# Performance work log

Measured on AMD Instinct MI355X. Metric: run time of the kernel, lower is better.

## Reference

```python
import jax, jax.numpy as jnp
import numpy as np
import math

N = 100000      # nodes
E = 1600000     # edges
F_IN = 256      # num_features
H = 64          # num_hidden
C = 64          # num_classes
L = 8           # num_layers
ALPHA = 0.5
THETA = 1.0


def setup_inputs() -> dict:
    key = jax.random.key(0)
    ks = jax.random.split(key, 7)
    x = jax.random.normal(ks[0], (N, F_IN), dtype=jnp.float32)
    edge_index = jax.random.randint(ks[1], (2, E), 0, N, dtype=jnp.int64)
    w_in = jax.random.normal(ks[2], (F_IN, H), dtype=jnp.float32) / np.float32(math.sqrt(F_IN))
    b_in = jnp.zeros((H,), dtype=jnp.float32)
    w_layers = jax.random.normal(ks[3], (L, H, H), dtype=jnp.float32) / np.float32(math.sqrt(H))
    w_out = jax.random.normal(ks[4], (H, C), dtype=jnp.float32) / np.float32(math.sqrt(H))
    b_out = jnp.zeros((C,), dtype=jnp.float32)
    return {"x": x, "edge_index": edge_index, "w_in": w_in, "b_in": b_in,
            "w_layers": w_layers, "w_out": w_out, "b_out": b_out}


def reference(x, edge_index, w_in, b_in, w_layers, w_out, b_out):
    # --- gcn_norm: add self loops, symmetric D^-1/2 (A+I) D^-1/2 ---
    loop = jnp.arange(N, dtype=edge_index.dtype)
    src = jnp.concatenate([edge_index[0], loop])   # [E+N]
    dst = jnp.concatenate([edge_index[1], loop])   # [E+N]
    deg = jax.ops.segment_sum(jnp.ones_like(src, dtype=x.dtype), dst, num_segments=N)
    dinv = jnp.where(deg > 0, jax.lax.rsqrt(jnp.maximum(deg, 1e-12)), 0.0)
    norm = dinv[src] * dinv[dst]                   # [E+N]

    # initial linear + ELU (dropout is identity in eval mode)
    h = jax.nn.elu(x @ w_in + b_in)                # [N, H]
    x0 = h

    for l in range(L):
        beta = math.log(THETA / (l + 1) + 1.0)     # GCN2Conv beta, layer index 1-based
        # sparse neighbor aggregation: P_hat @ h
        agg = jax.ops.segment_sum(norm[:, None] * h[src], dst, num_segments=N)  # [N, H]
        s = (1.0 - ALPHA) * agg + ALPHA * x0       # initial residual
        out = (1.0 - beta) * s + beta * (s @ w_layers[l])  # identity mapping (shared weights)
        h = jax.nn.elu(out) + out                  # elu + residual (dropout off)

    return h @ w_out + b_out                       # [N, C]
```

## Files before the change

kernel.cpp:

```cpp
#include <hip/hip_runtime.h>
#include <hip/hip_fp16.h>
#include <math.h>

#define NN 100000
#define EE 1600000
#define HH 64
#define LL 8
#define NBLK ((NN + 1023) / 1024)
#define AGG3_BLOCKS ((NN + 31) / 32)

#define NPB 512
#define BSH 9
#define NBUCK ((NN + NPB - 1) / NPB)
#define BIN_CHUNK 4096

typedef _Float16 f16x8 __attribute__((ext_vector_type(8)));
typedef float f32x4 __attribute__((ext_vector_type(4)));

__device__ __forceinline__ float eluf(float x) { return x > 0.0f ? x : expm1f(x); }


__global__ void count_edges_v2(const int* __restrict__ dst, int* __restrict__ counts) {
    int i = blockIdx.x * blockDim.x + threadIdx.x;
    if (i < EE) atomicAdd(&counts[dst[i]], 1);
}

__global__ void scan_block_v2(const int* __restrict__ counts, int* __restrict__ rp,
                              int* __restrict__ partial, float* __restrict__ dinv) {
    __shared__ int sm[256];
    const int t = threadIdx.x;
    const int base = blockIdx.x * 1024 + t * 4;
    int v0 = 0, v1 = 0, v2 = 0, v3 = 0;
    if (base + 0 < NN) v0 = counts[base + 0];
    if (base + 1 < NN) v1 = counts[base + 1];
    if (base + 2 < NN) v2 = counts[base + 2];
    if (base + 3 < NN) v3 = counts[base + 3];
    if (base + 0 < NN) dinv[base + 0] = rsqrtf((float)(v0 + 1));
    if (base + 1 < NN) dinv[base + 1] = rsqrtf((float)(v1 + 1));
    if (base + 2 < NN) dinv[base + 2] = rsqrtf((float)(v2 + 1));
    if (base + 3 < NN) dinv[base + 3] = rsqrtf((float)(v3 + 1));
    const int s = v0 + v1 + v2 + v3;
    sm[t] = s;
    __syncthreads();
    for (int off = 1; off < 256; off <<= 1) {
        int x = 0;
        if (t >= off) x = sm[t - off];
        __syncthreads();
        if (t >= off) sm[t] += x;
        __syncthreads();
    }
    int excl = sm[t] - s;
    if (t == 255) partial[blockIdx.x] = sm[255];
    if (base + 0 < NN) rp[base + 0] = excl;
    excl += v0;
    if (base + 1 < NN) rp[base + 1] = excl;
    excl += v1;
    if (base + 2 < NN) rp[base + 2] = excl;
    excl += v2;
    if (base + 3 < NN) rp[base + 3] = excl;
}

__global__ void scan_top_v2(int* partial) {
    __shared__ int sm[128];
    const int t = threadIdx.x;
    const int v = (t < NBLK) ? partial[t] : 0;
    sm[t] = v;
    __syncthreads();
    for (int off = 1; off < 128; off <<= 1) {
        int x = 0;
        if (t >= off) x = sm[t - off];
        __syncthreads();
        if (t >= off) sm[t] += x;
        __syncthreads();
    }
    if (t < NBLK) partial[t] = sm[t] - v;
}

__global__ void scan_add_v2(int* rp, const int* __restrict__ partial) {
    const int i = blockIdx.x * blockDim.x + threadIdx.x;
    if (i < NN) rp[i] += partial[i >> 10];
    else if (i == NN) rp[NN] = EE;
}


__global__ __launch_bounds__(256) void bin_edges_v1(const int* __restrict__ src,
                                                    const int* __restrict__ dst,
                                                    const int* __restrict__ rp,
                                                    int* __restrict__ bfill,
                                                    unsigned* __restrict__ tmp) {
    __shared__ int hist[NBUCK];
    __shared__ int basei[NBUCK];
    __shared__ int rpb[NBUCK];
    __shared__ int cur[NBUCK];
    const int t = threadIdx.x;
    const int e0 = blockIdx.x * BIN_CHUNK;
    for (int b = t; b < NBUCK; b += 256) {
        hist[b] = 0;
        cur[b] = 0;
    }
    __syncthreads();
    int myd[16];
#pragma unroll
    for (int i = 0; i < 16; ++i) {
        const int e = e0 + i * 256 + t;
        int d = -1;
        if (e < EE) {
            d = dst[e];
            atomicAdd(&hist[d >> BSH], 1);
        }
        myd[i] = d;
    }
    __syncthreads();
    for (int b = t; b < NBUCK; b += 256) {
        const int h = hist[b];
        basei[b] = h ? atomicAdd(&bfill[b], h) : 0;
        rpb[b] = rp[b << BSH];
    }
    __syncthreads();
#pragma unroll
    for (int i = 0; i < 16; ++i) {
        const int e = e0 + i * 256 + t;
        if (e < EE) {
            const int d = myd[i];
            const int b = d >> BSH;
            const int slot = atomicAdd(&cur[b], 1);
            tmp[rpb[b] + basei[b] + slot] =
                ((unsigned)(d & (NPB - 1)) << 17) | (unsigned)src[e];
        }
    }
}

__global__ __launch_bounds__(512) void unbin_v1(const unsigned* __restrict__ tmp,
                                                const int* __restrict__ rp,
                                                int* __restrict__ col) {
    __shared__ int lrp[NPB];
    __shared__ int lfill[NPB];
    const int t = threadIdx.x;
    const int node0 = blockIdx.x << BSH;
    const int nodes = (NN - node0 < NPB) ? (NN - node0) : NPB;
    for (int i = t; i < nodes; i += 512) {
        lrp[i] = rp[node0 + i];
        lfill[i] = 0;
    }
    __syncthreads();
    const int lo = rp[node0];
    const int hi = rp[node0 + nodes];
    for (int e = lo + t; e < hi; e += 512) {
        const unsigned v = tmp[e];
        const int s = (int)(v & 0x1FFFFu);
        const int doff = (int)(v >> 17);
        const int pos = lrp[doff] + atomicAdd(&lfill[doff], 1);
        col[pos] = s;
    }
}

__global__ void init_sent_v2(__half* a, __half* b) {
    const int t = threadIdx.x;
    if (t < 64) a[(size_t)NN * HH + t] = __float2half(0.f);
    else b[(size_t)NN * HH + (t - 64)] = __float2half(0.f);
}

__global__ void conv_w_v1(const float* __restrict__ w, __half* __restrict__ wt) {
    const int t = threadIdx.x;
    const int c = t & 63;
    const int k0 = (t >> 6) * 64;
    for (int k = 0; k < 64; ++k)
        wt[(size_t)c * 256 + k0 + k] = __float2half(w[(size_t)(k0 + k) * 64 + c]);
}

__global__ void conv_wbl_v1(const float* __restrict__ w_layers, __half* __restrict__ btab) {
    const int l = blockIdx.x;
    const float beta = logf(1.0f / (float)(l + 1) + 1.0f);
    const float* W = w_layers + (size_t)l * 64 * 64;
    __half* wt = btab + (size_t)l * 64 * 64;
    const int t = threadIdx.x;
    const int c = t & 63;
    const int k0 = (t >> 6) * 16;
    for (int k = k0; k < k0 + 16; ++k)
        wt[(size_t)c * 64 + k] = __float2half(beta * W[(size_t)k * 64 + c]);
}


__global__ __launch_bounds__(256) void agg_v3(
    const int* __restrict__ rp, const int* __restrict__ col, const float* __restrict__ dinv,
    const __half* __restrict__ hin, const float* __restrict__ x0, float* __restrict__ sout) {
    const int lane = threadIdx.x & 63;
    const int g = lane >> 3;
    const int fc = (lane & 7) << 3;
    const int wid = blockIdx.x * 4 + (threadIdx.x >> 6);
    const int node = wid * 8 + g;
    if (node >= NN) return;

    const int start = rp[node], end = rp[node + 1];
    float acc[8] = {};
    for (int e = start; e < end; e += 4) {
        const int c0 = col[e];
        const int c1 = (e + 1 < end) ? col[e + 1] : NN;
        const int c2 = (e + 2 < end) ? col[e + 2] : NN;
        const int c3 = (e + 3 < end) ? col[e + 3] : NN;
        float4 r0 = *(const float4*)(hin + ((size_t)c0 << 6) + fc);
        float4 r1 = *(const float4*)(hin + ((size_t)c1 << 6) + fc);
        float4 r2 = *(const float4*)(hin + ((size_t)c2 << 6) + fc);
        float4 r3 = *(const float4*)(hin + ((size_t)c3 << 6) + fc);
        const __half2* h0 = (const __half2*)&r0;
        const __half2* h1 = (const __half2*)&r1;
        const __half2* h2 = (const __half2*)&r2;
        const __half2* h3 = (const __half2*)&r3;
#pragma unroll
        for (int q = 0; q < 4; ++q) {
            const float2 f0 = __half22float2(h0[q]);
            const float2 f1 = __half22float2(h1[q]);
            const float2 f2 = __half22float2(h2[q]);
            const float2 f3 = __half22float2(h3[q]);
            acc[2 * q] += (f0.x + f1.x) + (f2.x + f3.x);
            acc[2 * q + 1] += (f0.y + f1.y) + (f2.y + f3.y);
        }
    }
    {
        float4 r = *(const float4*)(hin + ((size_t)node << 6) + fc);
        const __half2* hh = (const __half2*)&r;
#pragma unroll
        for (int q = 0; q < 4; ++q) {
            const float2 f = __half22float2(hh[q]);
            acc[2 * q] += f.x;
            acc[2 * q + 1] += f.y;
        }
        const float di = dinv[node];
        const float4* xp = (const float4*)(x0 + ((size_t)node << 6) + fc);
        const float4 xa = xp[0], xb = xp[1];
        float4 oa, ob;
        oa.x = 0.5f * fmaf(di, acc[0], xa.x);
        oa.y = 0.5f * fmaf(di, acc[1], xa.y);
        oa.z = 0.5f * fmaf(di, acc[2], xa.z);
        oa.w = 0.5f * fmaf(di, acc[3], xa.w);
        ob.x = 0.5f * fmaf(di, acc[4], xb.x);
        ob.y = 0.5f * fmaf(di, acc[5], xb.y);
        ob.z = 0.5f * fmaf(di, acc[6], xb.z);
        ob.w = 0.5f * fmaf(di, acc[7], xb.w);
        float4* sp = (float4*)(sout + ((size_t)node << 6) + fc);
        sp[0] = oa;
        sp[1] = ob;
    }
}


__global__ __launch_bounds__(256, 6) void mgemm_in_v2(
    const float* __restrict__ A, const __half* __restrict__ wt,
    const float* __restrict__ bias, const float* __restrict__ dinvp,
    float* __restrict__ out32, __half* __restrict__ out16) {
    __shared__ __half sh[64][136];
    const int t = threadIdx.x;
    const int row0 = blockIdx.x * 64;
    const int lane = t & 63;
    const int w = t >> 6;
    const int la = lane & 15, lg = lane >> 4;
    f32x4 acc[4] = {};

#pragma unroll
    for (int kh = 0; kh < 2; ++kh) {
#pragma unroll
        for (int i = 0; i < 8; ++i) {
            const int linear = t + i * 256;
            const int r = linear >> 5;
            const int q = linear & 31;
            const int grow = row0 + r;
            float4 v = make_float4(0.f, 0.f, 0.f, 0.f);
            if (grow < NN) v = *(const float4*)&A[(size_t)grow * 256 + kh * 128 + q * 4];
            __half2* dst = (__half2*)&sh[r][q * 4];
            dst[0] = __floats2half2_rn(v.x, v.y);
            dst[1] = __floats2half2_rn(v.z, v.w);
        }
        __syncthreads();
        const __half* arow = &sh[w * 16 + la][0];
#pragma unroll
        for (int kc = 0; kc < 4; ++kc) {
            const int k0 = kc * 32 + lg * 8;
            const f16x8 a = *(const f16x8*)&arow[k0];
#pragma unroll
            for (int tt = 0; tt < 4; ++tt) {
                const f16x8 b = *(const f16x8*)&wt[(size_t)(la + 16 * tt) * 256 + kh * 128 + k0];
                acc[tt] = __builtin_amdgcn_mfma_f32_16x16x32_f16(a, b, acc[tt], 0, 0, 0);
            }
        }
        __syncthreads();
    }

#pragma unroll
    for (int i = 0; i < 4; ++i) {
        const int r = row0 + w * 16 + lg * 4 + i;
        if (r >= NN) continue;
        const float dv = dinvp[r];
#pragma unroll
        for (int tt = 0; tt < 4; ++tt) {
            const int c = la + 16 * tt;
            float o = acc[tt][i] + bias[c];
            o = eluf(o);
            out32[(size_t)r * 64 + c] = o;
            out16[(size_t)r * 64 + c] = __float2half(o * dv);
        }
    }
}


__global__ __launch_bounds__(256, 8) void lgemm_v5(
    const float* __restrict__ S, const __half* __restrict__ wt, float obeta,
    const float* __restrict__ dinvp, __half* __restrict__ out16,
    float* __restrict__ out32, int w32) {
    __shared__ float sa[64][68];
    const int t = threadIdx.x;
    const int row0 = blockIdx.x * 64;

#pragma unroll
    for (int i = 0; i < 4; ++i) {
        const int linear = t + i * 256;
        const int r = linear >> 4, q = linear & 15;
        const int grow = row0 + r;
        float4 v = make_float4(0.f, 0.f, 0.f, 0.f);
        if (grow < NN) v = *(const float4*)&S[(size_t)grow * 64 + q * 4];
        *(float4*)&sa[r][q * 4] = v;
    }
    __syncthreads();

    const int lane = t & 63;
    const int w = t >> 6;
    const int la = lane & 15, lg = lane >> 4;
    f32x4 acc[4] = {};
    const float* arow = &sa[w * 16 + la][0];
#pragma unroll
    for (int kc = 0; kc < 2; ++kc) {
        const int k0 = kc * 32 + lg * 8;
        const float4 s0 = *(const float4*)&arow[k0];
        const float4 s1 = *(const float4*)&arow[k0 + 4];
        f16x8 a;
        a[0] = (_Float16)s0.x; a[1] = (_Float16)s0.y;
        a[2] = (_Float16)s0.z; a[3] = (_Float16)s0.w;
        a[4] = (_Float16)s1.x; a[5] = (_Float16)s1.y;
        a[6] = (_Float16)s1.z; a[7] = (_Float16)s1.w;
#pragma unroll
        for (int tt = 0; tt < 4; ++tt) {
            const f16x8 b = *(const f16x8*)&wt[(size_t)(la + 16 * tt) * 64 + k0];
            acc[tt] = __builtin_amdgcn_mfma_f32_16x16x32_f16(a, b, acc[tt], 0, 0, 0);
        }
    }

#pragma unroll
    for (int i = 0; i < 4; ++i) {
        const int lr = w * 16 + lg * 4 + i;
        const int r = row0 + lr;
        if (r >= NN) continue;
        const float dv = dinvp[r];
#pragma unroll
        for (int tt = 0; tt < 4; ++tt) {
            const int c = la + 16 * tt;
            const float o = acc[tt][i] + obeta * sa[lr][c];
            const float h = eluf(o) + o;
            out16[(size_t)r * 64 + c] = __float2half(h * dv);
            if (w32) out32[(size_t)r * 64 + c] = h;
        }
    }
}


template <int KTOT, int MODE>
__global__ __launch_bounds__(256, 4) void gemm_v2(const float* __restrict__ A,
                                                  const float* __restrict__ B,
                                                  const float* __restrict__ bias,
                                                  const float* __restrict__ dinvp,
                                                  float* __restrict__ out32,
                                                  __half* __restrict__ out16) {
    __shared__ float ss[64][68];
    __shared__ float ws[64][64];
    const int t = threadIdx.x;
    const int row0 = blockIdx.x * 64;
    const int tx = t & 15, ty = t >> 4;
    float acc[4][4] = {};

    for (int kc = 0; kc < KTOT; kc += 64) {
#pragma unroll
        for (int i = 0; i < 4; ++i) {
            const int linear = t + i * 256;
            const int r = linear >> 4, q = linear & 15;
            const int grow = row0 + r;
            float4 v = make_float4(0.f, 0.f, 0.f, 0.f);
            if (grow < NN) v = *(const float4*)&A[(size_t)grow * KTOT + kc + q * 4];
            *(float4*)&ss[r][q * 4] = v;
        }
#pragma unroll
        for (int i = 0; i < 4; ++i) {
            const int linear = t + i * 256;
            const int r = linear >> 4, q = linear & 15;
            *(float4*)&ws[r][q * 4] = *(const float4*)&B[(size_t)(kc + r) * 64 + q * 4];
        }
        __syncthreads();
#pragma unroll 4
        for (int k = 0; k < 64; k += 4) {
            float4 af[4], bf[4];
            af[0] = *(const float4*)&ss[ty * 4 + 0][k];
            af[1] = *(const float4*)&ss[ty * 4 + 1][k];
            af[2] = *(const float4*)&ss[ty * 4 + 2][k];
            af[3] = *(const float4*)&ss[ty * 4 + 3][k];
            bf[0] = *(const float4*)&ws[k + 0][tx * 4];
            bf[1] = *(const float4*)&ws[k + 1][tx * 4];
            bf[2] = *(const float4*)&ws[k + 2][tx * 4];
            bf[3] = *(const float4*)&ws[k + 3][tx * 4];
            const float* A4 = (const float*)af;
            const float* B4 = (const float*)bf;
#pragma unroll
            for (int i = 0; i < 4; ++i)
#pragma unroll
                for (int kk = 0; kk < 4; ++kk)
#pragma unroll
                    for (int j = 0; j < 4; ++j)
                        acc[i][j] = fmaf(A4[i * 4 + kk], B4[kk * 4 + j], acc[i][j]);
        }
        __syncthreads();
    }

#pragma unroll
    for (int i = 0; i < 4; ++i) {
        const int r = row0 + ty * 4 + i;
        if (r >= NN) continue;
        float4 o;
        float* op = (float*)&o;
#pragma unroll
        for (int j = 0; j < 4; ++j) {
            float xv = acc[i][j] + bias[tx * 4 + j];
            if (MODE == 0) xv = eluf(xv);
            op[j] = xv;
        }
        *(float4*)&out32[(size_t)r * 64 + tx * 4] = o;
        if (MODE == 0) {
            const float dv = dinvp[r];
            __half2* hp = (__half2*)&out16[(size_t)r * 64 + tx * 4];
            hp[0] = __floats2half2_rn(o.x * dv, o.y * dv);
            hp[1] = __floats2half2_rn(o.z * dv, o.w * dv);
        }
    }
}


extern "C" void kernel_launch(void* const* d_in, const int* in_sizes, int n_in, void* d_out,
                              int out_size, void* d_ws, size_t ws_size, hipStream_t stream) {
    const float* x = (const float*)d_in[0];
    const int* ei = (const int*)d_in[1];
    const float* w_in = (const float*)d_in[2];
    const float* b_in = (const float*)d_in[3];
    const float* w_layers = (const float*)d_in[4];
    const float* w_out = (const float*)d_in[5];
    const float* b_out = (const float*)d_in[6];
    float* out = (float*)d_out;

    char* p = (char*)d_ws;
    auto alloc = [&](size_t bytes) -> char* {
        char* r = p;
        p += (bytes + 255) & ~(size_t)255;
        return r;
    };
    int* counts = (int*)alloc((size_t)NN * 4);
    int* bfill = (int*)alloc((size_t)NBUCK * 4);
    int* rp = (int*)alloc((size_t)(NN + 1) * 4);
    int* partial = (int*)alloc(128 * 4);
    float* dinv = (float*)alloc((size_t)NN * 4);
    int* colA = (int*)alloc((size_t)EE * 4);
    unsigned* tmp = (unsigned*)alloc((size_t)EE * 4);
    float* x0 = (float*)alloc((size_t)NN * HH * 4);
    __half* x0h = (__half*)alloc((size_t)(NN + 1) * HH * 2);
    __half* hA = (__half*)alloc((size_t)(NN + 1) * HH * 2);
    float* sbuf = (float*)alloc((size_t)NN * HH * 4);
    __half* wt = (__half*)alloc((size_t)64 * 256 * 2);
    __half* btab = (__half*)alloc((size_t)LL * 64 * 64 * 2);

    const int* srcA = ei;
    const int* dstA = ei + EE;

    hipMemsetAsync(counts, 0, (size_t)NN * 4, stream);
    hipMemsetAsync(bfill, 0, (size_t)NBUCK * 4, stream);
    init_sent_v2<<<1, 128, 0, stream>>>(x0h, hA);
    conv_w_v1<<<1, 256, 0, stream>>>(w_in, wt);
    conv_wbl_v1<<<LL, 256, 0, stream>>>(w_layers, btab);
    count_edges_v2<<<(EE + 255) / 256, 256, 0, stream>>>(dstA, counts);
    scan_block_v2<<<NBLK, 256, 0, stream>>>(counts, rp, partial, dinv);
    scan_top_v2<<<1, 128, 0, stream>>>(partial);
    scan_add_v2<<<(NN + 1 + 255) / 256, 256, 0, stream>>>(rp, partial);
    bin_edges_v1<<<(EE + BIN_CHUNK - 1) / BIN_CHUNK, 256, 0, stream>>>(srcA, dstA, rp, bfill,
                                                                       tmp);
    unbin_v1<<<NBUCK, 512, 0, stream>>>(tmp, rp, colA);

    mgemm_in_v2<<<(NN + 63) / 64, 256, 0, stream>>>(x, wt, b_in, dinv, x0, x0h);

    for (int l = 0; l < LL; ++l) {
        const float obeta = 1.0f - (float)log(1.0 / (double)(l + 1) + 1.0);
        const __half* hin = (l & 1) ? hA : x0h;
        __half* hout = (l & 1) ? x0h : hA;
        agg_v3<<<AGG3_BLOCKS, 256, 0, stream>>>(rp, colA, dinv, hin, x0, sbuf);
        lgemm_v5<<<(NN + 63) / 64, 256, 0, stream>>>(sbuf, btab + (size_t)l * 64 * 64, obeta,
                                                     dinv, hout, sbuf, l == LL - 1);
    }
    gemm_v2<64, 2><<<(NN + 63) / 64, 256, 0, stream>>>(sbuf, w_out, b_out, nullptr, out, nullptr);
}
```

Measured before the change: 765.2 us.

## Fuse per-layer neighbor aggregation and layer GEMM into one kernel

Merges the gather-aggregation kernel and the per-layer MFMA GEMM into a single kernel. Each 256-thread block aggregates 64 nodes in two passes and keeps the aggregated rows in shared memory instead of writing them to a global fp32 buffer and reading them back. This drops one launch and a full N×64 fp32 round trip per layer. In exchange, the gather is now tied to 64-row blocks with a barrier before the GEMM, so degree imbalance within a block stalls the MFMA phase and occupancy may change.

```diff
diff --git a/kernel.cpp b/kernel.cpp
--- a/kernel.cpp
+++ b/kernel.cpp
@@ -7,7 +7,6 @@
 #define HH 64
 #define LL 8
 #define NBLK ((NN + 1023) / 1024)
-#define AGG3_BLOCKS ((NN + 31) / 32)
 
 #define NPB 512
 #define BSH 9
@@ -181,65 +180,112 @@
 }
 
 
-__global__ __launch_bounds__(256) void agg_v3(
+__global__ __launch_bounds__(256, 6) void fused_layer_v2(
     const int* __restrict__ rp, const int* __restrict__ col, const float* __restrict__ dinv,
-    const __half* __restrict__ hin, const float* __restrict__ x0, float* __restrict__ sout) {
-    const int lane = threadIdx.x & 63;
+    const __half* __restrict__ hin, const float* __restrict__ x0,
+    const __half* __restrict__ wt, float obeta,
+    __half* __restrict__ out16, float* __restrict__ out32, int w32) {
+    __shared__ float sa[64][68];
+    const int t = threadIdx.x;
+    const int row0 = blockIdx.x * 64;
+    const int lane = t & 63;
+    const int w = t >> 6;
     const int g = lane >> 3;
     const int fc = (lane & 7) << 3;
-    const int wid = blockIdx.x * 4 + (threadIdx.x >> 6);
-    const int node = wid * 8 + g;
-    if (node >= NN) return;
-
-    const int start = rp[node], end = rp[node + 1];
-    float acc[8] = {};
-    for (int e = start; e < end; e += 4) {
-        const int c0 = col[e];
-        const int c1 = (e + 1 < end) ? col[e + 1] : NN;
-        const int c2 = (e + 2 < end) ? col[e + 2] : NN;
-        const int c3 = (e + 3 < end) ? col[e + 3] : NN;
-        float4 r0 = *(const float4*)(hin + ((size_t)c0 << 6) + fc);
-        float4 r1 = *(const float4*)(hin + ((size_t)c1 << 6) + fc);
-        float4 r2 = *(const float4*)(hin + ((size_t)c2 << 6) + fc);
-        float4 r3 = *(const float4*)(hin + ((size_t)c3 << 6) + fc);
-        const __half2* h0 = (const __half2*)&r0;
-        const __half2* h1 = (const __half2*)&r1;
-        const __half2* h2 = (const __half2*)&r2;
-        const __half2* h3 = (const __half2*)&r3;
-#pragma unroll
-        for (int q = 0; q < 4; ++q) {
-            const float2 f0 = __half22float2(h0[q]);
-            const float2 f1 = __half22float2(h1[q]);
-            const float2 f2 = __half22float2(h2[q]);
-            const float2 f3 = __half22float2(h3[q]);
-            acc[2 * q] += (f0.x + f1.x) + (f2.x + f3.x);
-            acc[2 * q + 1] += (f0.y + f1.y) + (f2.y + f3.y);
-        }
-    }
-    {
-        float4 r = *(const float4*)(hin + ((size_t)node << 6) + fc);
-        const __half2* hh = (const __half2*)&r;
-#pragma unroll
-        for (int q = 0; q < 4; ++q) {
-            const float2 f = __half22float2(hh[q]);
-            acc[2 * q] += f.x;
-            acc[2 * q + 1] += f.y;
-        }
-        const float di = dinv[node];
-        const float4* xp = (const float4*)(x0 + ((size_t)node << 6) + fc);
-        const float4 xa = xp[0], xb = xp[1];
-        float4 oa, ob;
-        oa.x = 0.5f * fmaf(di, acc[0], xa.x);
-        oa.y = 0.5f * fmaf(di, acc[1], xa.y);
-        oa.z = 0.5f * fmaf(di, acc[2], xa.z);
-        oa.w = 0.5f * fmaf(di, acc[3], xa.w);
-        ob.x = 0.5f * fmaf(di, acc[4], xb.x);
-        ob.y = 0.5f * fmaf(di, acc[5], xb.y);
-        ob.z = 0.5f * fmaf(di, acc[6], xb.z);
-        ob.w = 0.5f * fmaf(di, acc[7], xb.w);
-        float4* sp = (float4*)(sout + ((size_t)node << 6) + fc);
-        sp[0] = oa;
-        sp[1] = ob;
+
+#pragma unroll
+    for (int pass = 0; pass < 2; ++pass) {
+        const int lrow = w * 16 + pass * 8 + g;
+        const int node = row0 + lrow;
+        float acc[8] = {};
+        if (node < NN) {
+            const int start = rp[node], end = rp[node + 1];
+            for (int e = start; e < end; e += 4) {
+                const int c0 = col[e];
+                const int c1 = (e + 1 < end) ? col[e + 1] : NN;
+                const int c2 = (e + 2 < end) ? col[e + 2] : NN;
+                const int c3 = (e + 3 < end) ? col[e + 3] : NN;
+                float4 r0 = *(const float4*)(hin + ((size_t)c0 << 6) + fc);
+                float4 r1 = *(const float4*)(hin + ((size_t)c1 << 6) + fc);
+                float4 r2 = *(const float4*)(hin + ((size_t)c2 << 6) + fc);
+                float4 r3 = *(const float4*)(hin + ((size_t)c3 << 6) + fc);
+                const __half2* h0 = (const __half2*)&r0;
+                const __half2* h1 = (const __half2*)&r1;
+                const __half2* h2 = (const __half2*)&r2;
+                const __half2* h3 = (const __half2*)&r3;
+#pragma unroll
+                for (int q = 0; q < 4; ++q) {
+                    const float2 f0 = __half22float2(h0[q]);
+                    const float2 f1 = __half22float2(h1[q]);
+                    const float2 f2 = __half22float2(h2[q]);
+                    const float2 f3 = __half22float2(h3[q]);
+                    acc[2 * q] += (f0.x + f1.x) + (f2.x + f3.x);
+                    acc[2 * q + 1] += (f0.y + f1.y) + (f2.y + f3.y);
+                }
+            }
+            float4 r = *(const float4*)(hin + ((size_t)node << 6) + fc);
+            const __half2* hh = (const __half2*)&r;
+#pragma unroll
+            for (int q = 0; q < 4; ++q) {
+                const float2 f = __half22float2(hh[q]);
+                acc[2 * q] += f.x;
+                acc[2 * q + 1] += f.y;
+            }
+            const float di = dinv[node];
+            const float4* xp = (const float4*)(x0 + ((size_t)node << 6) + fc);
+            const float4 xa = xp[0], xb = xp[1];
+            float4 oa, ob;
+            oa.x = 0.5f * fmaf(di, acc[0], xa.x);
+            oa.y = 0.5f * fmaf(di, acc[1], xa.y);
+            oa.z = 0.5f * fmaf(di, acc[2], xa.z);
+            oa.w = 0.5f * fmaf(di, acc[3], xa.w);
+            ob.x = 0.5f * fmaf(di, acc[4], xb.x);
+            ob.y = 0.5f * fmaf(di, acc[5], xb.y);
+            ob.z = 0.5f * fmaf(di, acc[6], xb.z);
+            ob.w = 0.5f * fmaf(di, acc[7], xb.w);
+            *(float4*)&sa[lrow][fc] = oa;
+            *(float4*)&sa[lrow][fc + 4] = ob;
+        } else {
+            *(float4*)&sa[lrow][fc] = make_float4(0.f, 0.f, 0.f, 0.f);
+            *(float4*)&sa[lrow][fc + 4] = make_float4(0.f, 0.f, 0.f, 0.f);
+        }
+    }
+    __syncthreads();
+
+    const int la = lane & 15, lg = lane >> 4;
+    f32x4 acc2[4] = {};
+    const float* arow = &sa[w * 16 + la][0];
+#pragma unroll
+    for (int kc = 0; kc < 2; ++kc) {
+        const int k0 = kc * 32 + lg * 8;
+        const float4 s0 = *(const float4*)&arow[k0];
+        const float4 s1 = *(const float4*)&arow[k0 + 4];
+        f16x8 a;
+        a[0] = (_Float16)s0.x; a[1] = (_Float16)s0.y;
+        a[2] = (_Float16)s0.z; a[3] = (_Float16)s0.w;
+        a[4] = (_Float16)s1.x; a[5] = (_Float16)s1.y;
+        a[6] = (_Float16)s1.z; a[7] = (_Float16)s1.w;
+#pragma unroll
+        for (int tt = 0; tt < 4; ++tt) {
+            const f16x8 b = *(const f16x8*)&wt[(size_t)(la + 16 * tt) * 64 + k0];
+            acc2[tt] = __builtin_amdgcn_mfma_f32_16x16x32_f16(a, b, acc2[tt], 0, 0, 0);
+        }
+    }
+
+#pragma unroll
+    for (int i = 0; i < 4; ++i) {
+        const int lr = w * 16 + lg * 4 + i;
+        const int r = row0 + lr;
+        if (r >= NN) continue;
+        const float dv = dinv[r];
+#pragma unroll
+        for (int tt = 0; tt < 4; ++tt) {
+            const int c = la + 16 * tt;
+            const float o = acc2[tt][i] + obeta * sa[lr][c];
+            const float h = eluf(o) + o;
+            out16[(size_t)r * 64 + c] = __float2half(h * dv);
+            if (w32) out32[(size_t)r * 64 + c] = h;
+        }
     }
 }
 
@@ -297,65 +343,6 @@
             o = eluf(o);
             out32[(size_t)r * 64 + c] = o;
             out16[(size_t)r * 64 + c] = __float2half(o * dv);
-        }
-    }
-}
-
-
-__global__ __launch_bounds__(256, 8) void lgemm_v5(
-    const float* __restrict__ S, const __half* __restrict__ wt, float obeta,
-    const float* __restrict__ dinvp, __half* __restrict__ out16,
-    float* __restrict__ out32, int w32) {
-    __shared__ float sa[64][68];
-    const int t = threadIdx.x;
-    const int row0 = blockIdx.x * 64;
-
-#pragma unroll
-    for (int i = 0; i < 4; ++i) {
-        const int linear = t + i * 256;
-        const int r = linear >> 4, q = linear & 15;
-        const int grow = row0 + r;
-        float4 v = make_float4(0.f, 0.f, 0.f, 0.f);
-        if (grow < NN) v = *(const float4*)&S[(size_t)grow * 64 + q * 4];
-        *(float4*)&sa[r][q * 4] = v;
-    }
-    __syncthreads();
-
-    const int lane = t & 63;
-    const int w = t >> 6;
-    const int la = lane & 15, lg = lane >> 4;
-    f32x4 acc[4] = {};
-    const float* arow = &sa[w * 16 + la][0];
-#pragma unroll
-    for (int kc = 0; kc < 2; ++kc) {
-        const int k0 = kc * 32 + lg * 8;
-        const float4 s0 = *(const float4*)&arow[k0];
-        const float4 s1 = *(const float4*)&arow[k0 + 4];
-        f16x8 a;
-        a[0] = (_Float16)s0.x; a[1] = (_Float16)s0.y;
-        a[2] = (_Float16)s0.z; a[3] = (_Float16)s0.w;
-        a[4] = (_Float16)s1.x; a[5] = (_Float16)s1.y;
-        a[6] = (_Float16)s1.z; a[7] = (_Float16)s1.w;
-#pragma unroll
-        for (int tt = 0; tt < 4; ++tt) {
-            const f16x8 b = *(const f16x8*)&wt[(size_t)(la + 16 * tt) * 64 + k0];
-            acc[tt] = __builtin_amdgcn_mfma_f32_16x16x32_f16(a, b, acc[tt], 0, 0, 0);
-        }
-    }
-
-#pragma unroll
-    for (int i = 0; i < 4; ++i) {
-        const int lr = w * 16 + lg * 4 + i;
-        const int r = row0 + lr;
-        if (r >= NN) continue;
-        const float dv = dinvp[r];
-#pragma unroll
-        for (int tt = 0; tt < 4; ++tt) {
-            const int c = la + 16 * tt;
-            const float o = acc[tt][i] + obeta * sa[lr][c];
-            const float h = eluf(o) + o;
-            out16[(size_t)r * 64 + c] = __float2half(h * dv);
-            if (w32) out32[(size_t)r * 64 + c] = h;
         }
     }
 }
@@ -492,9 +479,9 @@
         const float obeta = 1.0f - (float)log(1.0 / (double)(l + 1) + 1.0);
         const __half* hin = (l & 1) ? hA : x0h;
         __half* hout = (l & 1) ? x0h : hA;
-        agg_v3<<<AGG3_BLOCKS, 256, 0, stream>>>(rp, colA, dinv, hin, x0, sbuf);
-        lgemm_v5<<<(NN + 63) / 64, 256, 0, stream>>>(sbuf, btab + (size_t)l * 64 * 64, obeta,
-                                                     dinv, hout, sbuf, l == LL - 1);
+        fused_layer_v2<<<(NN + 63) / 64, 256, 0, stream>>>(
+            rp, colA, dinv, hin, x0, btab + (size_t)l * 64 * 64, obeta, hout, sbuf,
+            l == LL - 1);
     }
     gemm_v2<64, 2><<<(NN + 63) / 64, 256, 0, stream>>>(sbuf, w_out, b_out, nullptr, out, nullptr);
 }
```

Measured after the change: 689.8 us. -9.9%, faster.
